# Kernel optimization log

Measured on AMD Instinct MI355X. Metric: run time of the kernel, lower is better.

## Reference

```python
import jax, jax.numpy as jnp
import numpy as np

IMAGE_SIZE = 1024
STRIDE = 16        # encode_stride
KERNEL = 21        # encode_kernel (gaussian sigma)
MASK = 64          # attn_mask_size
TWO_SIGMA2 = 2.0 * KERNEL * KERNEL  # 882; gaussian center offset 3*21+1 = 64


def setup_inputs() -> dict:
    key = jax.random.key(0)
    k1, k2 = jax.random.split(key)
    B, P = 256, 32
    # pixel-space coordinates in [0, image_size)
    boxes = jax.random.uniform(k1, (B, 4), dtype=jnp.float32) * IMAGE_SIZE
    point_coords = jax.random.uniform(k2, (B, P, 2), dtype=jnp.float32) * IMAGE_SIZE
    return {"boxes": boxes, "point_coords": point_coords}


def reference(boxes, point_coords):
    # Coordinates are quantized with int() (trunc); inputs are non-negative so floor == trunc.
    grid = jnp.arange(MASK)  # [64] shared row/col coordinate vector

    # ---------------- bbox_attn_mask (binary box splat) ----------------
    x0, y0, x1, y1 = boxes[:, 0], boxes[:, 1], boxes[:, 2], boxes[:, 3]
    xmin = jnp.minimum(x0, x1); xmax = jnp.maximum(x0, x1)
    ymin = jnp.minimum(y0, y1); ymax = jnp.maximum(y0, y1)
    q = lambda v: jnp.floor(v / STRIDE).astype(jnp.int32)
    xmin_i = jnp.maximum(q(xmin), 0)
    ymin_i = jnp.maximum(q(ymin), 0)
    xmax_i = jnp.minimum(q(xmax) + 1, MASK)   # exclusive
    ymax_i = jnp.minimum(q(ymax) + 1, MASK)
    in_x = (grid[None, :] >= xmin_i[:, None]) & (grid[None, :] < xmax_i[:, None])  # [B, W]
    in_y = (grid[None, :] >= ymin_i[:, None]) & (grid[None, :] < ymax_i[:, None])  # [B, H]
    bbox_mask = (in_y[:, :, None] & in_x[:, None, :]).astype(jnp.float32)          # [B, 64, 64]

    # ---------------- point_attn_mask (gaussian splat, max-combine) ----------------
    # Original slices a precomputed 129x129 gaussian g[a,b] = exp(-((a-64)^2+(b-64)^2)/(2*sigma^2))
    # centered at the quantized point; since the kernel half-width (64) covers the whole 64x64
    # grid for any in-range point, the splat equals the analytic gaussian over the full grid.
    px = jnp.floor(point_coords[..., 0] / STRIDE).astype(jnp.int32)  # [B, P]
    py = jnp.floor(point_coords[..., 1] / STRIDE).astype(jnp.int32)
    valid = (px >= 0) & (py >= 0) & (px < MASK) & (py < MASK)        # [B, P]
    dj = grid[None, None, None, :] - px[:, :, None, None]            # [B, P, 1, 64]
    di = grid[None, None, :, None] - py[:, :, None, None]            # [B, P, 64, 1]
    d2 = (di * di + dj * dj).astype(jnp.float32)                     # [B, P, 64, 64]
    g = jnp.exp(-d2 / TWO_SIGMA2)
    g = jnp.where(valid[:, :, None, None], g, 0.0)                   # skip out-of-range points
    point_mask = jnp.max(g, axis=1)                                  # max-combine over points; zeros init

    return bbox_mask, point_mask
```

## Files before the change

### kernel.cpp

```cpp
#include <hip/hip_runtime.h>
#include <math.h>

#define MASKN 64
#define NPTS 32
#define INV_STRIDE 0.0625f
#define NEG_INV_TWO_SIGMA2 (-1.0f / 882.0f)

__global__ __launch_bounds__(256) void fused_masks_kernel(
    const float* __restrict__ boxes,
    const float* __restrict__ pts,
    float* __restrict__ out_bbox,
    float* __restrict__ out_point)
{
    const int b = blockIdx.x;
    const int t = threadIdx.x;

    __shared__ float rf[NPTS][MASKN];
    __shared__ float cf[NPTS][MASKN];
    __shared__ int   s_px[NPTS];
    __shared__ int   s_py[NPTS];
    __shared__ int   s_valid[NPTS];
    __shared__ int   s_box[4];

    if (t < NPTS) {
        float x = pts[((size_t)b * NPTS + t) * 2 + 0];
        float y = pts[((size_t)b * NPTS + t) * 2 + 1];
        int px = (int)floorf(x * INV_STRIDE);
        int py = (int)floorf(y * INV_STRIDE);
        s_px[t] = px;
        s_py[t] = py;
        s_valid[t] = (px >= 0) && (py >= 0) && (px < MASKN) && (py < MASKN);
    }
    if (t == 0) {
        float x0 = boxes[b * 4 + 0], y0 = boxes[b * 4 + 1];
        float x1 = boxes[b * 4 + 2], y1 = boxes[b * 4 + 3];
        float xmn = fminf(x0, x1), xmx = fmaxf(x0, x1);
        float ymn = fminf(y0, y1), ymx = fmaxf(y0, y1);
        int xmin_i = max((int)floorf(xmn * INV_STRIDE), 0);
        int xmax_i = min((int)floorf(xmx * INV_STRIDE) + 1, MASKN);
        int ymin_i = max((int)floorf(ymn * INV_STRIDE), 0);
        int ymax_i = min((int)floorf(ymx * INV_STRIDE) + 1, MASKN);
        s_box[0] = xmin_i; s_box[1] = xmax_i;
        s_box[2] = ymin_i; s_box[3] = ymax_i;
    }
    __syncthreads();

    for (int e = t; e < NPTS * MASKN; e += 256) {
        int p = e >> 6, i = e & 63;
        float v = s_valid[p] ? 1.0f : 0.0f;
        float dy = (float)(i - s_py[p]);
        float dx = (float)(i - s_px[p]);
        rf[p][i] = v * __expf(dy * dy * NEG_INV_TWO_SIGMA2);
        cf[p][i] = v * __expf(dx * dx * NEG_INV_TWO_SIGMA2);
    }
    __syncthreads();

    const int xmin_i = s_box[0], xmax_i = s_box[1];
    const int ymin_i = s_box[2], ymax_i = s_box[3];

    const int j0 = (t & 15) * 4;
    const int r0 = t >> 4;

    float4 m[4];
    #pragma unroll
    for (int k = 0; k < 4; ++k) m[k] = make_float4(0.f, 0.f, 0.f, 0.f);

    for (int p = 0; p < NPTS; ++p) {
        const float4 c = *(const float4*)&cf[p][j0];
        #pragma unroll
        for (int k = 0; k < 4; ++k) {
            const float ry = rf[p][r0 + 16 * k];
            m[k].x = fmaxf(m[k].x, ry * c.x);
            m[k].y = fmaxf(m[k].y, ry * c.y);
            m[k].z = fmaxf(m[k].z, ry * c.z);
            m[k].w = fmaxf(m[k].w, ry * c.w);
        }
    }

    const size_t base = (size_t)b * (MASKN * MASKN);
    const float bx0 = (j0 + 0 >= xmin_i && j0 + 0 < xmax_i) ? 1.0f : 0.0f;
    const float bx1 = (j0 + 1 >= xmin_i && j0 + 1 < xmax_i) ? 1.0f : 0.0f;
    const float bx2 = (j0 + 2 >= xmin_i && j0 + 2 < xmax_i) ? 1.0f : 0.0f;
    const float bx3 = (j0 + 3 >= xmin_i && j0 + 3 < xmax_i) ? 1.0f : 0.0f;

    #pragma unroll
    for (int k = 0; k < 4; ++k) {
        const int i = r0 + 16 * k;
        const int idx = i * MASKN + j0;
        *(float4*)&out_point[base + idx] = m[k];
        const float iny = (i >= ymin_i && i < ymax_i) ? 1.0f : 0.0f;
        float4 bb = make_float4(iny * bx0, iny * bx1, iny * bx2, iny * bx3);
        *(float4*)&out_bbox[base + idx] = bb;
    }
}

extern "C" void kernel_launch(void* const* d_in, const int* in_sizes, int n_in,
                              void* d_out, int out_size, void* d_ws, size_t ws_size,
                              hipStream_t stream) {
    const float* boxes = (const float*)d_in[0];
    const float* pts   = (const float*)d_in[1];
    float* out = (float*)d_out;

    const int B = in_sizes[0] / 4;
    float* out_bbox  = out;
    float* out_point = out + (size_t)B * MASKN * MASKN;

    fused_masks_kernel<<<dim3(B), dim3(256), 0, stream>>>(boxes, pts, out_bbox, out_point);
}
```

Baseline: 60.63 us.

## Split each batch image across two blocks and drop the preamble sync

Launches two blocks per batch item, each covering half of the 64 rows, so the grid has 512 blocks instead of 256 and spreads better over the CUs. Each thread now loads point coordinates straight from global memory inside the separable-factor loop, and every thread computes the box bounds itself, which removes the shared-memory staging step and one barrier. Each thread accumulates two adjacent rows using float2 row loads. The cost is that both blocks recompute the full 32x64 row and column factor tables, and global loads are repeated across threads.

Result: no change. 59.73 us (-1.5%).

```diff
diff --git a/kernel.cpp b/kernel.cpp
--- a/kernel.cpp
+++ b/kernel.cpp
@@ -6,75 +6,60 @@
 #define INV_STRIDE 0.0625f
 #define NEG_INV_TWO_SIGMA2 (-1.0f / 882.0f)
 
-__global__ __launch_bounds__(256) void fused_masks_kernel(
+__global__ __launch_bounds__(256, 2) void fused_masks_kernel(
     const float* __restrict__ boxes,
     const float* __restrict__ pts,
     float* __restrict__ out_bbox,
     float* __restrict__ out_point)
 {
-    const int b = blockIdx.x;
-    const int t = threadIdx.x;
+    const int b       = blockIdx.x >> 1;
+    const int rowbase = (blockIdx.x & 1) * (MASKN / 2);
+    const int t       = threadIdx.x;
 
     __shared__ float rf[NPTS][MASKN];
     __shared__ float cf[NPTS][MASKN];
-    __shared__ int   s_px[NPTS];
-    __shared__ int   s_py[NPTS];
-    __shared__ int   s_valid[NPTS];
-    __shared__ int   s_box[4];
-
-    if (t < NPTS) {
-        float x = pts[((size_t)b * NPTS + t) * 2 + 0];
-        float y = pts[((size_t)b * NPTS + t) * 2 + 1];
-        int px = (int)floorf(x * INV_STRIDE);
-        int py = (int)floorf(y * INV_STRIDE);
-        s_px[t] = px;
-        s_py[t] = py;
-        s_valid[t] = (px >= 0) && (py >= 0) && (px < MASKN) && (py < MASKN);
-    }
-    if (t == 0) {
-        float x0 = boxes[b * 4 + 0], y0 = boxes[b * 4 + 1];
-        float x1 = boxes[b * 4 + 2], y1 = boxes[b * 4 + 3];
-        float xmn = fminf(x0, x1), xmx = fmaxf(x0, x1);
-        float ymn = fminf(y0, y1), ymx = fmaxf(y0, y1);
-        int xmin_i = max((int)floorf(xmn * INV_STRIDE), 0);
-        int xmax_i = min((int)floorf(xmx * INV_STRIDE) + 1, MASKN);
-        int ymin_i = max((int)floorf(ymn * INV_STRIDE), 0);
-        int ymax_i = min((int)floorf(ymx * INV_STRIDE) + 1, MASKN);
-        s_box[0] = xmin_i; s_box[1] = xmax_i;
-        s_box[2] = ymin_i; s_box[3] = ymax_i;
-    }
-    __syncthreads();
 
     for (int e = t; e < NPTS * MASKN; e += 256) {
-        int p = e >> 6, i = e & 63;
-        float v = s_valid[p] ? 1.0f : 0.0f;
-        float dy = (float)(i - s_py[p]);
-        float dx = (float)(i - s_px[p]);
+        const int p = e >> 6;
+        const int i = e & 63;
+        const float x = pts[((size_t)b * NPTS + p) * 2 + 0];
+        const float y = pts[((size_t)b * NPTS + p) * 2 + 1];
+        const int px = (int)floorf(x * INV_STRIDE);
+        const int py = (int)floorf(y * INV_STRIDE);
+        const float v = (px >= 0 && py >= 0 && px < MASKN && py < MASKN) ? 1.0f : 0.0f;
+        const float dy = (float)(i - py);
+        const float dx = (float)(i - px);
         rf[p][i] = v * __expf(dy * dy * NEG_INV_TWO_SIGMA2);
         cf[p][i] = v * __expf(dx * dx * NEG_INV_TWO_SIGMA2);
     }
+
+    const float x0 = boxes[b * 4 + 0], y0 = boxes[b * 4 + 1];
+    const float x1 = boxes[b * 4 + 2], y1 = boxes[b * 4 + 3];
+    const int xmin_i = max((int)floorf(fminf(x0, x1) * INV_STRIDE), 0);
+    const int xmax_i = min((int)floorf(fmaxf(x0, x1) * INV_STRIDE) + 1, MASKN);
+    const int ymin_i = max((int)floorf(fminf(y0, y1) * INV_STRIDE), 0);
+    const int ymax_i = min((int)floorf(fmaxf(y0, y1) * INV_STRIDE) + 1, MASKN);
+
     __syncthreads();
 
-    const int xmin_i = s_box[0], xmax_i = s_box[1];
-    const int ymin_i = s_box[2], ymax_i = s_box[3];
+    const int j0 = (t & 15) * 4;
+    const int r0 = rowbase + (t >> 4) * 2;
 
-    const int j0 = (t & 15) * 4;
-    const int r0 = t >> 4;
+    float4 m0 = make_float4(0.f, 0.f, 0.f, 0.f);
+    float4 m1 = make_float4(0.f, 0.f, 0.f, 0.f);
 
-    float4 m[4];
-    #pragma unroll
-    for (int k = 0; k < 4; ++k) m[k] = make_float4(0.f, 0.f, 0.f, 0.f);
-
+    #pragma unroll 4
     for (int p = 0; p < NPTS; ++p) {
-        const float4 c = *(const float4*)&cf[p][j0];
-        #pragma unroll
-        for (int k = 0; k < 4; ++k) {
-            const float ry = rf[p][r0 + 16 * k];
-            m[k].x = fmaxf(m[k].x, ry * c.x);
-            m[k].y = fmaxf(m[k].y, ry * c.y);
-            m[k].z = fmaxf(m[k].z, ry * c.z);
-            m[k].w = fmaxf(m[k].w, ry * c.w);
-        }
+        const float4 c  = *(const float4*)&cf[p][j0];
+        const float2 ry = *(const float2*)&rf[p][r0];
+        m0.x = fmaxf(m0.x, ry.x * c.x);
+        m0.y = fmaxf(m0.y, ry.x * c.y);
+        m0.z = fmaxf(m0.z, ry.x * c.z);
+        m0.w = fmaxf(m0.w, ry.x * c.w);
+        m1.x = fmaxf(m1.x, ry.y * c.x);
+        m1.y = fmaxf(m1.y, ry.y * c.y);
+        m1.z = fmaxf(m1.z, ry.y * c.z);
+        m1.w = fmaxf(m1.w, ry.y * c.w);
     }
 
     const size_t base = (size_t)b * (MASKN * MASKN);
@@ -83,15 +68,14 @@
     const float bx2 = (j0 + 2 >= xmin_i && j0 + 2 < xmax_i) ? 1.0f : 0.0f;
     const float bx3 = (j0 + 3 >= xmin_i && j0 + 3 < xmax_i) ? 1.0f : 0.0f;
 
-    #pragma unroll
-    for (int k = 0; k < 4; ++k) {
-        const int i = r0 + 16 * k;
-        const int idx = i * MASKN + j0;
-        *(float4*)&out_point[base + idx] = m[k];
-        const float iny = (i >= ymin_i && i < ymax_i) ? 1.0f : 0.0f;
-        float4 bb = make_float4(iny * bx0, iny * bx1, iny * bx2, iny * bx3);
-        *(float4*)&out_bbox[base + idx] = bb;
-    }
+    const int   idx0 = r0 * MASKN + j0;
+    const float iny0 = (r0 + 0 >= ymin_i && r0 + 0 < ymax_i) ? 1.0f : 0.0f;
+    const float iny1 = (r0 + 1 >= ymin_i && r0 + 1 < ymax_i) ? 1.0f : 0.0f;
+
+    *(float4*)&out_point[base + idx0]         = m0;
+    *(float4*)&out_point[base + idx0 + MASKN] = m1;
+    *(float4*)&out_bbox[base + idx0]          = make_float4(iny0 * bx0, iny0 * bx1, iny0 * bx2, iny0 * bx3);
+    *(float4*)&out_bbox[base + idx0 + MASKN]  = make_float4(iny1 * bx0, iny1 * bx1, iny1 * bx2, iny1 * bx3);
 }
 
 extern "C" void kernel_launch(void* const* d_in, const int* in_sizes, int n_in,
@@ -105,5 +89,5 @@
     float* out_bbox  = out;
     float* out_point = out + (size_t)B * MASKN * MASKN;
 
-    fused_masks_kernel<<<dim3(B), dim3(256), 0, stream>>>(boxes, pts, out_bbox, out_point);
+    fused_masks_kernel<<<dim3(2 * B), dim3(256), 0, stream>>>(boxes, pts, out_bbox, out_point);
 }
```
